# Kernel tuning notes

Hardware: AMD Instinct MI355X
Metric: run time of the kernel (lower is better)

## Reference

```python
import jax, jax.numpy as jnp
import numpy as np

T_HORIZON, S_DIM, A_DIM, H = 65536, 128, 8, 256
GAMMA, LMBDA, EPS_CLIP, VF_COEF, ENT_COEF = 0.99, 0.95, 0.2, 0.5, 0.01
LOG2PI = float(np.log(2.0 * np.pi))


def setup_inputs() -> dict:
    key = jax.random.key(0)
    ks = jax.random.split(key, 24)
    s = jax.random.normal(ks[0], (T_HORIZON, S_DIM), jnp.float32)
    a = jax.random.normal(ks[1], (T_HORIZON, A_DIM), jnp.float32)
    r = jax.random.normal(ks[2], (T_HORIZON, 1), jnp.float32)
    sp = jax.random.normal(ks[3], (T_HORIZON, S_DIM), jnp.float32)
    log_prob_a_old = jax.random.normal(ks[4], (T_HORIZON, 1), jnp.float32)
    d_mask = (jax.random.uniform(ks[5], (T_HORIZON, 1)) > 0.05).astype(jnp.float32)

    def lin(k, fan_in, fan_out, std):
        return jax.random.normal(k, (fan_in, fan_out), jnp.float32) * (std / np.sqrt(fan_in))

    params = dict(
        pi_W1=lin(ks[6], S_DIM, H, np.sqrt(2)), pi_b1=jnp.zeros((H,), jnp.float32),
        pi_W2=lin(ks[7], H, H, np.sqrt(2)),     pi_b2=jnp.zeros((H,), jnp.float32),
        mu_W=lin(ks[8], H, A_DIM, 0.01),        mu_b=jnp.zeros((A_DIM,), jnp.float32),
        log_std=jnp.zeros((A_DIM,), jnp.float32),
        v_W1=lin(ks[9], S_DIM, H, np.sqrt(2)),  v_b1=jnp.zeros((H,), jnp.float32),
        v_W2=lin(ks[10], H, H, np.sqrt(2)),     v_b2=jnp.zeros((H,), jnp.float32),
        vh_W=lin(ks[11], H, 1, 1.0),            vh_b=jnp.zeros((1,), jnp.float32),
    )
    return dict(s=s, a=a, r=r, sp=sp, log_prob_a_old=log_prob_a_old, d_mask=d_mask, **params)


def reference(s, a, r, sp, log_prob_a_old, d_mask,
              pi_W1, pi_b1, pi_W2, pi_b2, mu_W, mu_b, log_std,
              v_W1, v_b1, v_W2, v_b2, vh_W, vh_b):
    def mlp(x, W1, b1, W2, b2):
        return jnp.tanh(jnp.tanh(x @ W1 + b1) @ W2 + b2)

    def v_fn(x):
        return mlp(x, v_W1, v_b1, v_W2, v_b2) @ vh_W + vh_b  # [N, 1]

    # ---- GAE (computed under no_grad in the original) ----
    values = jax.lax.stop_gradient(v_fn(s))                  # [T, 1]
    v_last = jax.lax.stop_gradient(v_fn(sp[-1:]))            # [1, 1]
    next_values = jnp.concatenate([values[1:], v_last], axis=0)
    deltas = r + GAMMA * next_values * d_mask - values       # [T, 1]

    def gae_step(gae, inp):
        delta, m = inp
        gae = delta + GAMMA * LMBDA * m * gae
        return gae, gae

    _, advantages = jax.lax.scan(gae_step, jnp.zeros((1,), deltas.dtype),
                                 (deltas, d_mask), reverse=True)  # [T, 1]
    returns = advantages + values
    advantages = (advantages - advantages.mean()) / (advantages.std(ddof=1) + 1e-8)
    advantages = jax.lax.stop_gradient(advantages)
    returns = jax.lax.stop_gradient(returns)

    # ---- PPO clipped loss (single full-batch pass) ----
    mu = mlp(s, pi_W1, pi_b1, pi_W2, pi_b2) @ mu_W + mu_b    # [T, A]
    std = jnp.exp(log_std)
    log_prob = (-0.5 * ((a - mu) / std) ** 2 - log_std - 0.5 * LOG2PI).sum(-1, keepdims=True)
    ratio = jnp.exp(log_prob - log_prob_a_old)               # [T, 1]
    pg_loss = -jnp.minimum(ratio * advantages,
                           jnp.clip(ratio, 1.0 - EPS_CLIP, 1.0 + EPS_CLIP) * advantages).mean()
    diff = v_fn(s) - returns
    vf_loss = jnp.where(jnp.abs(diff) < 1.0, 0.5 * diff ** 2, jnp.abs(diff) - 0.5).mean()
    entropy = (0.5 + 0.5 * LOG2PI + log_std).mean()          # Normal entropy, constant over batch
    return pg_loss + VF_COEF * vf_loss - ENT_COEF * entropy
```

## Files before the change

kernel.cpp:

```cpp
#include <hip/hip_runtime.h>
#include <math.h>

#define TH 65536
#define SD 128
#define AD 8
#define HD 256

constexpr float GAMMA  = 0.99f;
constexpr float LMBDA  = 0.95f;
constexpr float EPSC   = 0.2f;
constexpr float VFC    = 0.5f;
constexpr float ENTC   = 0.01f;
constexpr float LOG2PI = 1.8378770664093453f;

typedef __attribute__((ext_vector_type(8))) short short8;
typedef __attribute__((ext_vector_type(4))) float f32x4;

constexpr size_t WS_VALUES = 0;
constexpr size_t WS_ADV    = 65540;
constexpr size_t WS_RATIO  = 131080;
constexpr size_t WS_CHP    = 196616;
constexpr size_t WS_CHB    = 196680;
constexpr size_t WS_CARRY  = 196744;
constexpr size_t WS_SCAL   = 196808;
constexpr size_t WS_BF     = 196816;
constexpr size_t SW_PIW1 = 0;
constexpr size_t SW_PIW2 = 32768;
constexpr size_t SW_VW1  = 98304;
constexpr size_t SW_VW2  = 131072;

__device__ __forceinline__ unsigned short f2bf(float x) {
    unsigned int u = __float_as_uint(x);
    unsigned int r = (u + 0x7fffu + ((u >> 16) & 1u)) >> 16;
    return (unsigned short)r;
}

__device__ __forceinline__ float ftanh(float x) {
    float cx = fminf(fmaxf(x, -9.f), 9.f);
    float e = __expf(cx + cx);
    return (e - 1.f) * __builtin_amdgcn_rcpf(e + 1.f);
}

__global__ __launch_bounds__(256) void swizzle_kernel(
    const float* __restrict__ piW1, const float* __restrict__ vW1,
    const float* __restrict__ piW2, const float* __restrict__ vW2,
    unsigned short* __restrict__ dPiW1, unsigned short* __restrict__ dVW1,
    unsigned short* __restrict__ dPiW2, unsigned short* __restrict__ dVW2,
    float* __restrict__ scal)
{
    if (blockIdx.x == 0 && threadIdx.x < 8) scal[threadIdx.x] = 0.f;
    int fid = blockIdx.x * 256 + threadIdx.x;
    const float* S; unsigned short* D; int lo;
    if      (fid <  4096) { S = piW1; D = dPiW1; lo = 0;     }
    else if (fid <  8192) { S = vW1;  D = dVW1;  lo = 4096;  }
    else if (fid < 16384) { S = piW2; D = dPiW2; lo = 8192;  }
    else                  { S = vW2;  D = dVW2;  lo = 16384; }
    int f = fid - lo;
    int lane = f & 63, grp = f >> 6;
    int nt = grp % 16, ks = grp / 16;
    int k0 = ks * 32 + ((lane >> 4) << 3);
    int n  = nt * 16 + (lane & 15);
    unsigned int u[4];
#pragma unroll
    for (int jj = 0; jj < 4; ++jj) {
        float v0 = S[(size_t)(k0 + 2 * jj) * HD + n];
        float v1 = S[(size_t)(k0 + 2 * jj + 1) * HD + n];
        u[jj] = (unsigned int)f2bf(v0) | ((unsigned int)f2bf(v1) << 16);
    }
    ((uint4*)D)[f] = make_uint4(u[0], u[1], u[2], u[3]);
}

template <int NKS, int ASTRIDE>
__device__ __forceinline__ void runlayer(
    f32x4* acc, const unsigned short* __restrict__ Ws,
    const unsigned short* ab, int l15, int quad, int rowgrp, int colhalf, int lane)
{
#pragma unroll
    for (int nt = 0; nt < 8; ++nt) acc[nt] = (f32x4){0.f, 0.f, 0.f, 0.f};
#pragma unroll
    for (int ks = 0; ks < NKS; ++ks) {
        short8 af = *(const short8*)(ab + (rowgrp * 16 + l15) * ASTRIDE + ks * 32 + quad * 8);
#pragma unroll
        for (int ntl = 0; ntl < 8; ++ntl) {
            short8 bf = ((const short8*)Ws)[(ks * 16 + colhalf * 8 + ntl) * 64 + lane];
            acc[ntl] = __builtin_amdgcn_mfma_f32_16x16x32_bf16(af, bf, acc[ntl], 0, 0, 0);
        }
    }
}

__global__ __launch_bounds__(256, 3) void mlp_fused_kernel(
    const float* __restrict__ X, const float* __restrict__ Xlast,
    const unsigned short* __restrict__ piW1s, const float* __restrict__ pib1,
    const unsigned short* __restrict__ piW2s, const float* __restrict__ pib2,
    const float* __restrict__ muW, const float* __restrict__ mub,
    const float* __restrict__ logstd,
    const float* __restrict__ act, const float* __restrict__ lpold,
    const unsigned short* __restrict__ vW1s, const float* __restrict__ vb1,
    const unsigned short* __restrict__ vW2s, const float* __restrict__ vb2,
    const float* __restrict__ vhW, const float* __restrict__ vhb,
    float* __restrict__ values, float* __restrict__ ratio)
{
    __shared__ unsigned short xs[32 * 136];
    __shared__ unsigned short h1[32 * 264];
    __shared__ float cmb[2][32][8];
    const int tid = threadIdx.x;
    const int lane = tid & 63, wave = tid >> 6;
    const int l15 = lane & 15, quad = lane >> 4;
    const int rowgrp = wave >> 1, colhalf = wave & 1;
    const bool vonly = (blockIdx.x == gridDim.x - 1);
    const float* Xp = vonly ? Xlast : X + (size_t)blockIdx.x * 32 * SD;
    const int nrows = vonly ? 1 : 32;
    const int vout0 = vonly ? TH : blockIdx.x * 32;

#pragma unroll
    for (int i = 0; i < 4; ++i) {
        int f = tid + i * 256;
        int rr = f >> 5, c4 = f & 31;
        float4 v = make_float4(0.f, 0.f, 0.f, 0.f);
        if (rr < nrows) v = *(const float4*)(Xp + (size_t)rr * SD + c4 * 4);
        unsigned int u0 = (unsigned int)f2bf(v.x) | ((unsigned int)f2bf(v.y) << 16);
        unsigned int u1 = (unsigned int)f2bf(v.z) | ((unsigned int)f2bf(v.w) << 16);
        *(uint2*)(xs + rr * 136 + c4 * 4) = make_uint2(u0, u1);
    }
    __syncthreads();

    f32x4 acc[8];

    if (!vonly) {
        runlayer<4, 136>(acc, piW1s, xs, l15, quad, rowgrp, colhalf, lane);
#pragma unroll
        for (int ntl = 0; ntl < 8; ++ntl) {
            int col = (colhalf * 8 + ntl) * 16 + l15;
            float bb = pib1[col];
#pragma unroll
            for (int rg = 0; rg < 4; ++rg)
                h1[(rowgrp * 16 + quad * 4 + rg) * 264 + col] = f2bf(ftanh(acc[ntl][rg] + bb));
        }
        __syncthreads();
        runlayer<8, 264>(acc, piW2s, h1, l15, quad, rowgrp, colhalf, lane);
        float pm[4][8];
#pragma unroll
        for (int rg = 0; rg < 4; ++rg)
#pragma unroll
            for (int aj = 0; aj < 8; ++aj) pm[rg][aj] = 0.f;
#pragma unroll
        for (int ntl = 0; ntl < 8; ++ntl) {
            int col = (colhalf * 8 + ntl) * 16 + l15;
            float bb = pib2[col];
            float4 w0 = *(const float4*)(muW + (size_t)col * AD);
            float4 w1 = *(const float4*)(muW + (size_t)col * AD + 4);
            float wv[8] = {w0.x, w0.y, w0.z, w0.w, w1.x, w1.y, w1.z, w1.w};
#pragma unroll
            for (int rg = 0; rg < 4; ++rg) {
                float hv = ftanh(acc[ntl][rg] + bb);
#pragma unroll
                for (int aj = 0; aj < 8; ++aj) pm[rg][aj] = fmaf(hv, wv[aj], pm[rg][aj]);
            }
        }
#pragma unroll
        for (int off = 8; off >= 1; off >>= 1)
#pragma unroll
            for (int rg = 0; rg < 4; ++rg)
#pragma unroll
                for (int aj = 0; aj < 8; ++aj)
                    pm[rg][aj] += __shfl_xor(pm[rg][aj], off, 16);
        if (l15 == 0) {
#pragma unroll
            for (int rg = 0; rg < 4; ++rg) {
                *(float4*)&cmb[colhalf][rowgrp * 16 + quad * 4 + rg][0] =
                    make_float4(pm[rg][0], pm[rg][1], pm[rg][2], pm[rg][3]);
                *(float4*)&cmb[colhalf][rowgrp * 16 + quad * 4 + rg][4] =
                    make_float4(pm[rg][4], pm[rg][5], pm[rg][6], pm[rg][7]);
            }
        }
        __syncthreads();
        if (tid < 32) {
            int row = blockIdx.x * 32 + tid;
            const float* ar = act + (size_t)row * AD;
            float lp = 0.f;
#pragma unroll
            for (int aj = 0; aj < 8; ++aj) {
                float ls = logstd[aj];
                float mu = cmb[0][tid][aj] + cmb[1][tid][aj] + mub[aj];
                float z = (ar[aj] - mu) * __expf(-ls);
                lp += -0.5f * z * z - ls;
            }
            lp -= 4.f * LOG2PI;
            ratio[row] = __expf(lp - lpold[row]);
        }
    }

    runlayer<4, 136>(acc, vW1s, xs, l15, quad, rowgrp, colhalf, lane);
#pragma unroll
    for (int ntl = 0; ntl < 8; ++ntl) {
        int col = (colhalf * 8 + ntl) * 16 + l15;
        float bb = vb1[col];
#pragma unroll
        for (int rg = 0; rg < 4; ++rg)
            h1[(rowgrp * 16 + quad * 4 + rg) * 264 + col] = f2bf(ftanh(acc[ntl][rg] + bb));
    }
    __syncthreads();
    runlayer<8, 264>(acc, vW2s, h1, l15, quad, rowgrp, colhalf, lane);
    float vp[4] = {0.f, 0.f, 0.f, 0.f};
#pragma unroll
    for (int ntl = 0; ntl < 8; ++ntl) {
        int col = (colhalf * 8 + ntl) * 16 + l15;
        float bb = vb2[col], w = vhW[col];
#pragma unroll
        for (int rg = 0; rg < 4; ++rg) vp[rg] += ftanh(acc[ntl][rg] + bb) * w;
    }
#pragma unroll
    for (int off = 8; off >= 1; off >>= 1)
#pragma unroll
        for (int rg = 0; rg < 4; ++rg) vp[rg] += __shfl_xor(vp[rg], off, 16);
    if (l15 == 0) {
#pragma unroll
        for (int rg = 0; rg < 4; ++rg)
            cmb[colhalf][rowgrp * 16 + quad * 4 + rg][0] = vp[rg];
    }
    __syncthreads();
    if (tid < nrows)
        values[vout0 + tid] = cmb[0][tid][0] + cmb[1][tid][0] + vhb[0];
}

__global__ __launch_bounds__(256) void gae_chunk_kernel(
    const float* __restrict__ rw, const float* __restrict__ m,
    const float* __restrict__ values,
    float* __restrict__ chunkP, float* __restrict__ chunkB)
{
    __shared__ float sp_[256], sb_[256];
    const int j = threadIdx.x;
    const int t0 = blockIdx.x * 1024 + j * 4;

    float4 vv = *(const float4*)(values + t0);
    float v4 = values[t0 + 4];
    float4 rr = *(const float4*)(rw + t0);
    float4 mm = *(const float4*)(m + t0);
    float vs[5] = {vv.x, vv.y, vv.z, vv.w, v4};
    float rs[4] = {rr.x, rr.y, rr.z, rr.w};
    float ms[4] = {mm.x, mm.y, mm.z, mm.w};
    float d[4];
#pragma unroll
    for (int i = 0; i < 4; ++i)
        d[i] = rs[i] + GAMMA * vs[i + 1] * ms[i] - vs[i];

    const float g = GAMMA * LMBDA;
    float P = 1.f, B = 0.f;
#pragma unroll
    for (int i = 3; i >= 0; --i) {
        float p = g * ms[i];
        B = d[i] + p * B;
        P = p * P;
    }
    sp_[j] = P; sb_[j] = B;
    __syncthreads();
    for (int dstep = 1; dstep < 256; dstep <<= 1) {
        float pj = sp_[j], bj = sb_[j], pk = 1.f, bk = 0.f;
        if (j + dstep < 256) { pk = sp_[j + dstep]; bk = sb_[j + dstep]; }
        __syncthreads();
        sp_[j] = pj * pk;
        sb_[j] = bj + pj * bk;
        __syncthreads();
    }
    if (j == 0) { chunkP[blockIdx.x] = sp_[0]; chunkB[blockIdx.x] = sb_[0]; }
}

__global__ __launch_bounds__(64) void gae_carry_kernel(
    const float* __restrict__ chunkP, const float* __restrict__ chunkB,
    float* __restrict__ carry)
{
    if (threadIdx.x == 0) {
        float A = 0.f;
        for (int c = 63; c >= 0; --c) {
            carry[c] = A;
            A = chunkB[c] + chunkP[c] * A;
        }
    }
}

__global__ __launch_bounds__(256) void gae_apply_kernel(
    const float* __restrict__ rw, const float* __restrict__ m,
    const float* __restrict__ values, const float* __restrict__ carry,
    float* __restrict__ adv_out, float* __restrict__ scal)
{
    __shared__ float sp_[256], sb_[256];
    __shared__ float red[12];
    const int j = threadIdx.x;
    const int t0 = blockIdx.x * 1024 + j * 4;

    float4 vv = *(const float4*)(values + t0);
    float v4 = values[t0 + 4];
    float4 rr = *(const float4*)(rw + t0);
    float4 mm = *(const float4*)(m + t0);
    float vs[5] = {vv.x, vv.y, vv.z, vv.w, v4};
    float rs[4] = {rr.x, rr.y, rr.z, rr.w};
    float ms[4] = {mm.x, mm.y, mm.z, mm.w};
    float ds[4];
#pragma unroll
    for (int i = 0; i < 4; ++i)
        ds[i] = rs[i] + GAMMA * vs[i + 1] * ms[i] - vs[i];
    const float g = GAMMA * LMBDA;

    float P = 1.f, B = 0.f;
#pragma unroll
    for (int i = 3; i >= 0; --i) {
        float p = g * ms[i];
        B = ds[i] + p * B;
        P = p * P;
    }
    sp_[j] = P; sb_[j] = B;
    __syncthreads();
    for (int dstep = 1; dstep < 256; dstep <<= 1) {
        float pj = sp_[j], bj = sb_[j], pk = 1.f, bk = 0.f;
        if (j + dstep < 256) { pk = sp_[j + dstep]; bk = sb_[j + dstep]; }
        __syncthreads();
        sp_[j] = pj * pk;
        sb_[j] = bj + pj * bk;
        __syncthreads();
    }
    float Pe = 1.f, Be = 0.f;
    if (j < 255) { Pe = sp_[j + 1]; Be = sb_[j + 1]; }
    float A = Be + Pe * carry[blockIdx.x];

    float s1 = 0.f, s2 = 0.f, vf = 0.f;
    float a4[4];
#pragma unroll
    for (int i = 3; i >= 0; --i) {
        A = ds[i] + g * ms[i] * A;
        a4[i] = A;
        float ab = fabsf(A);
        vf += (ab < 1.f) ? 0.5f * A * A : ab - 0.5f;
        s1 += A;
        s2 += A * A;
    }
    *(float4*)(adv_out + t0) = make_float4(a4[0], a4[1], a4[2], a4[3]);

#pragma unroll
    for (int off = 32; off >= 1; off >>= 1) {
        s1 += __shfl_down(s1, off, 64);
        s2 += __shfl_down(s2, off, 64);
        vf += __shfl_down(vf, off, 64);
    }
    if ((j & 63) == 0) {
        int w = j >> 6;
        red[w] = s1; red[4 + w] = s2; red[8 + w] = vf;
    }
    __syncthreads();
    if (j == 0) {
        atomicAdd(&scal[0], red[0] + red[1] + red[2] + red[3]);
        atomicAdd(&scal[1], red[4] + red[5] + red[6] + red[7]);
        atomicAdd(&scal[2], red[8] + red[9] + red[10] + red[11]);
    }
}

__global__ __launch_bounds__(256) void pg_final_kernel(
    const float* __restrict__ ratio, const float* __restrict__ adv,
    float* __restrict__ scal, const float* __restrict__ logstd,
    float* __restrict__ out)
{
    __shared__ float red[4];
    const int tid = threadIdx.x;
    const int t0 = blockIdx.x * 1024 + tid * 4;

    const float ssum = scal[0], ssq = scal[1];
    const float meanA = ssum / (float)TH;
    const float varA = fmaxf((ssq - ssum * ssum / (float)TH) / (float)(TH - 1), 0.f);
    const float inv = 1.f / (sqrtf(varA) + 1e-8f);

    float4 a4 = *(const float4*)(adv + t0);
    float4 r4 = *(const float4*)(ratio + t0);
    float as[4] = {a4.x, a4.y, a4.z, a4.w};
    float rs[4] = {r4.x, r4.y, r4.z, r4.w};
    float pg = 0.f;
#pragma unroll
    for (int i = 0; i < 4; ++i) {
        float aN = (as[i] - meanA) * inv;
        float rc = fminf(fmaxf(rs[i], 1.f - EPSC), 1.f + EPSC);
        pg -= fminf(rs[i] * aN, rc * aN);
    }
#pragma unroll
    for (int off = 32; off >= 1; off >>= 1) pg += __shfl_down(pg, off, 64);
    if ((tid & 63) == 0) red[tid >> 6] = pg;
    __syncthreads();
    if (tid == 0) {
        atomicAdd(&scal[3], red[0] + red[1] + red[2] + red[3]);
        __threadfence();
        float old = atomicAdd(&scal[4], 1.f);
        if (old == 63.f) {
            float pgs = atomicAdd(&scal[3], 0.f);
            float vfs = atomicAdd(&scal[2], 0.f);
            float ls = 0.f;
#pragma unroll
            for (int jj = 0; jj < AD; ++jj) ls += logstd[jj];
            float entropy = 0.5f + 0.5f * LOG2PI + ls / (float)AD;
            out[0] = pgs / (float)TH + VFC * (vfs / (float)TH) - ENTC * entropy;
        }
    }
}

extern "C" void kernel_launch(void* const* d_in, const int* in_sizes, int n_in,
                              void* d_out, int out_size, void* d_ws, size_t ws_size,
                              hipStream_t stream) {
    const float* s      = (const float*)d_in[0];
    const float* a      = (const float*)d_in[1];
    const float* r      = (const float*)d_in[2];
    const float* sp     = (const float*)d_in[3];
    const float* lpold  = (const float*)d_in[4];
    const float* dmask  = (const float*)d_in[5];
    const float* piW1   = (const float*)d_in[6];
    const float* pib1   = (const float*)d_in[7];
    const float* piW2   = (const float*)d_in[8];
    const float* pib2   = (const float*)d_in[9];
    const float* muW    = (const float*)d_in[10];
    const float* mub    = (const float*)d_in[11];
    const float* logstd = (const float*)d_in[12];
    const float* vW1    = (const float*)d_in[13];
    const float* vb1    = (const float*)d_in[14];
    const float* vW2    = (const float*)d_in[15];
    const float* vb2    = (const float*)d_in[16];
    const float* vhW    = (const float*)d_in[17];
    const float* vhb    = (const float*)d_in[18];

    float* ws      = (float*)d_ws;
    float* values  = ws + WS_VALUES;
    float* adv     = ws + WS_ADV;
    float* ratio   = ws + WS_RATIO;
    float* chunkP  = ws + WS_CHP;
    float* chunkB  = ws + WS_CHB;
    float* carry   = ws + WS_CARRY;
    float* scal    = ws + WS_SCAL;
    unsigned short* bfbase = (unsigned short*)(ws + WS_BF);
    unsigned short* dPiW1 = bfbase + SW_PIW1;
    unsigned short* dPiW2 = bfbase + SW_PIW2;
    unsigned short* dVW1  = bfbase + SW_VW1;
    unsigned short* dVW2  = bfbase + SW_VW2;

    swizzle_kernel<<<96, 256, 0, stream>>>(piW1, vW1, piW2, vW2,
                                           dPiW1, dVW1, dPiW2, dVW2, scal);

    mlp_fused_kernel<<<TH / 32 + 1, 256, 0, stream>>>(
        s, sp + (size_t)(TH - 1) * SD,
        dPiW1, pib1, dPiW2, pib2, muW, mub, logstd, a, lpold,
        dVW1, vb1, dVW2, vb2, vhW, vhb,
        values, ratio);

    gae_chunk_kernel<<<64, 256, 0, stream>>>(r, dmask, values, chunkP, chunkB);
    gae_carry_kernel<<<1, 64, 0, stream>>>(chunkP, chunkB, carry);
    gae_apply_kernel<<<64, 256, 0, stream>>>(r, dmask, values, carry, adv, scal);

    pg_final_kernel<<<64, 256, 0, stream>>>(ratio, adv, scal, logstd, (float*)d_out);
}
```

Baseline: 207.1 us.

## Switch MFMA to fp16, coalesce weight swizzle, fuse GAE and loss kernels

Four post-MLP kernels (chunk scan, carry, apply, pg-final) are merged into one 64-block kernel that uses global atomic counters with spin-waits as grid barriers, which removes launch gaps and the advantage round-trip through memory. The MLP switches from bf16 to fp16 MFMA with packed round-toward-zero conversion. The weight swizzle is rewritten to read coalesced float4 rows and scatter 16-bit stores across twice as many blocks. The spin barriers assume all 64 blocks are resident at once, and fp16 changes numerical range and rounding.

```diff
diff --git a/kernel.cpp b/kernel.cpp
--- a/kernel.cpp
+++ b/kernel.cpp
@@ -13,26 +13,24 @@
 constexpr float ENTC   = 0.01f;
 constexpr float LOG2PI = 1.8378770664093453f;
 
-typedef __attribute__((ext_vector_type(8))) short short8;
+typedef _Float16 half8 __attribute__((ext_vector_type(8)));
+typedef __fp16 fp16x2 __attribute__((ext_vector_type(2)));
 typedef __attribute__((ext_vector_type(4))) float f32x4;
 
 constexpr size_t WS_VALUES = 0;
-constexpr size_t WS_ADV    = 65540;
 constexpr size_t WS_RATIO  = 131080;
 constexpr size_t WS_CHP    = 196616;
 constexpr size_t WS_CHB    = 196680;
-constexpr size_t WS_CARRY  = 196744;
-constexpr size_t WS_SCAL   = 196808;
-constexpr size_t WS_BF     = 196816;
+constexpr size_t WS_SCAL   = 196744;
+constexpr size_t WS_BF     = 196752;
 constexpr size_t SW_PIW1 = 0;
 constexpr size_t SW_PIW2 = 32768;
 constexpr size_t SW_VW1  = 98304;
 constexpr size_t SW_VW2  = 131072;
 
-__device__ __forceinline__ unsigned short f2bf(float x) {
-    unsigned int u = __float_as_uint(x);
-    unsigned int r = (u + 0x7fffu + ((u >> 16) & 1u)) >> 16;
-    return (unsigned short)r;
+__device__ __forceinline__ unsigned pk2h(float a, float b) {
+    fp16x2 h = __builtin_amdgcn_cvt_pkrtz(a, b);
+    return __builtin_bit_cast(unsigned, h);
 }
 
 __device__ __forceinline__ float ftanh(float x) {
@@ -49,25 +47,24 @@
     float* __restrict__ scal)
 {
     if (blockIdx.x == 0 && threadIdx.x < 8) scal[threadIdx.x] = 0.f;
-    int fid = blockIdx.x * 256 + threadIdx.x;
+    int g = blockIdx.x * 256 + threadIdx.x;
     const float* S; unsigned short* D; int lo;
-    if      (fid <  4096) { S = piW1; D = dPiW1; lo = 0;     }
-    else if (fid <  8192) { S = vW1;  D = dVW1;  lo = 4096;  }
-    else if (fid < 16384) { S = piW2; D = dPiW2; lo = 8192;  }
-    else                  { S = vW2;  D = dVW2;  lo = 16384; }
-    int f = fid - lo;
-    int lane = f & 63, grp = f >> 6;
-    int nt = grp % 16, ks = grp / 16;
-    int k0 = ks * 32 + ((lane >> 4) << 3);
-    int n  = nt * 16 + (lane & 15);
-    unsigned int u[4];
-#pragma unroll
-    for (int jj = 0; jj < 4; ++jj) {
-        float v0 = S[(size_t)(k0 + 2 * jj) * HD + n];
-        float v1 = S[(size_t)(k0 + 2 * jj + 1) * HD + n];
-        u[jj] = (unsigned int)f2bf(v0) | ((unsigned int)f2bf(v1) << 16);
-    }
-    ((uint4*)D)[f] = make_uint4(u[0], u[1], u[2], u[3]);
+    if      (g <  8192) { S = piW1; D = dPiW1; lo = 0;     }
+    else if (g < 24576) { S = piW2; D = dPiW2; lo = 8192;  }
+    else if (g < 32768) { S = vW1;  D = dVW1;  lo = 24576; }
+    else                { S = vW2;  D = dVW2;  lo = 32768; }
+    int q = g - lo;
+    int k = q >> 6, n4 = (q & 63) * 4;
+    float4 v = *(const float4*)(S + (size_t)k * HD + n4);
+    int ks = k >> 5, kq = (k >> 3) & 3, j = k & 7;
+    int nt = n4 >> 4, nr = n4 & 15;
+    unsigned short* base = D + ((size_t)(ks * 16 + nt) * 64 + kq * 16 + nr) * 8 + j;
+    unsigned p01 = pk2h(v.x, v.y);
+    unsigned p23 = pk2h(v.z, v.w);
+    base[0]  = (unsigned short)(p01 & 0xffff);
+    base[8]  = (unsigned short)(p01 >> 16);
+    base[16] = (unsigned short)(p23 & 0xffff);
+    base[24] = (unsigned short)(p23 >> 16);
 }
 
 template <int NKS, int ASTRIDE>
@@ -79,13 +76,23 @@
     for (int nt = 0; nt < 8; ++nt) acc[nt] = (f32x4){0.f, 0.f, 0.f, 0.f};
 #pragma unroll
     for (int ks = 0; ks < NKS; ++ks) {
-        short8 af = *(const short8*)(ab + (rowgrp * 16 + l15) * ASTRIDE + ks * 32 + quad * 8);
+        half8 af = *(const half8*)(ab + (rowgrp * 16 + l15) * ASTRIDE + ks * 32 + quad * 8);
 #pragma unroll
         for (int ntl = 0; ntl < 8; ++ntl) {
-            short8 bf = ((const short8*)Ws)[(ks * 16 + colhalf * 8 + ntl) * 64 + lane];
-            acc[ntl] = __builtin_amdgcn_mfma_f32_16x16x32_bf16(af, bf, acc[ntl], 0, 0, 0);
-        }
-    }
+            half8 bf = ((const half8*)Ws)[(ks * 16 + colhalf * 8 + ntl) * 64 + lane];
+            acc[ntl] = __builtin_amdgcn_mfma_f32_16x16x32_f16(af, bf, acc[ntl], 0, 0, 0);
+        }
+    }
+}
+
+__device__ __forceinline__ void store4(unsigned short* dst, int stride,
+                                       float t0, float t1, float t2, float t3)
+{
+    unsigned p01 = pk2h(t0, t1), p23 = pk2h(t2, t3);
+    dst[0]          = (unsigned short)(p01 & 0xffff);
+    dst[stride]     = (unsigned short)(p01 >> 16);
+    dst[2 * stride] = (unsigned short)(p23 & 0xffff);
+    dst[3 * stride] = (unsigned short)(p23 >> 16);
 }
 
 __global__ __launch_bounds__(256, 3) void mlp_fused_kernel(
@@ -118,9 +125,7 @@
         int rr = f >> 5, c4 = f & 31;
         float4 v = make_float4(0.f, 0.f, 0.f, 0.f);
         if (rr < nrows) v = *(const float4*)(Xp + (size_t)rr * SD + c4 * 4);
-        unsigned int u0 = (unsigned int)f2bf(v.x) | ((unsigned int)f2bf(v.y) << 16);
-        unsigned int u1 = (unsigned int)f2bf(v.z) | ((unsigned int)f2bf(v.w) << 16);
-        *(uint2*)(xs + rr * 136 + c4 * 4) = make_uint2(u0, u1);
+        *(uint2*)(xs + rr * 136 + c4 * 4) = make_uint2(pk2h(v.x, v.y), pk2h(v.z, v.w));
     }
     __syncthreads();
 
@@ -132,9 +137,9 @@
         for (int ntl = 0; ntl < 8; ++ntl) {
             int col = (colhalf * 8 + ntl) * 16 + l15;
             float bb = pib1[col];
-#pragma unroll
-            for (int rg = 0; rg < 4; ++rg)
-                h1[(rowgrp * 16 + quad * 4 + rg) * 264 + col] = f2bf(ftanh(acc[ntl][rg] + bb));
+            store4(&h1[(rowgrp * 16 + quad * 4) * 264 + col], 264,
+                   ftanh(acc[ntl][0] + bb), ftanh(acc[ntl][1] + bb),
+                   ftanh(acc[ntl][2] + bb), ftanh(acc[ntl][3] + bb));
         }
         __syncthreads();
         runlayer<8, 264>(acc, piW2s, h1, l15, quad, rowgrp, colhalf, lane);
@@ -195,9 +200,9 @@
     for (int ntl = 0; ntl < 8; ++ntl) {
         int col = (colhalf * 8 + ntl) * 16 + l15;
         float bb = vb1[col];
-#pragma unroll
-        for (int rg = 0; rg < 4; ++rg)
-            h1[(rowgrp * 16 + quad * 4 + rg) * 264 + col] = f2bf(ftanh(acc[ntl][rg] + bb));
+        store4(&h1[(rowgrp * 16 + quad * 4) * 264 + col], 264,
+               ftanh(acc[ntl][0] + bb), ftanh(acc[ntl][1] + bb),
+               ftanh(acc[ntl][2] + bb), ftanh(acc[ntl][3] + bb));
     }
     __syncthreads();
     runlayer<8, 264>(acc, vW2s, h1, l15, quad, rowgrp, colhalf, lane);
@@ -223,70 +228,20 @@
         values[vout0 + tid] = cmb[0][tid][0] + cmb[1][tid][0] + vhb[0];
 }
 
-__global__ __launch_bounds__(256) void gae_chunk_kernel(
+__global__ __launch_bounds__(256) void gae_fused_kernel(
     const float* __restrict__ rw, const float* __restrict__ m,
-    const float* __restrict__ values,
-    float* __restrict__ chunkP, float* __restrict__ chunkB)
+    const float* __restrict__ values, const float* __restrict__ ratio,
+    const float* __restrict__ logstd,
+    float* __restrict__ chunkP, float* __restrict__ chunkB,
+    float* __restrict__ scal, float* __restrict__ out)
 {
     __shared__ float sp_[256], sb_[256];
+    __shared__ float cp[64], cb[64];
+    __shared__ float red[12];
+    __shared__ float bcast[4];
     const int j = threadIdx.x;
     const int t0 = blockIdx.x * 1024 + j * 4;
-
-    float4 vv = *(const float4*)(values + t0);
-    float v4 = values[t0 + 4];
-    float4 rr = *(const float4*)(rw + t0);
-    float4 mm = *(const float4*)(m + t0);
-    float vs[5] = {vv.x, vv.y, vv.z, vv.w, v4};
-    float rs[4] = {rr.x, rr.y, rr.z, rr.w};
-    float ms[4] = {mm.x, mm.y, mm.z, mm.w};
-    float d[4];
-#pragma unroll
-    for (int i = 0; i < 4; ++i)
-        d[i] = rs[i] + GAMMA * vs[i + 1] * ms[i] - vs[i];
-
     const float g = GAMMA * LMBDA;
-    float P = 1.f, B = 0.f;
-#pragma unroll
-    for (int i = 3; i >= 0; --i) {
-        float p = g * ms[i];
-        B = d[i] + p * B;
-        P = p * P;
-    }
-    sp_[j] = P; sb_[j] = B;
-    __syncthreads();
-    for (int dstep = 1; dstep < 256; dstep <<= 1) {
-        float pj = sp_[j], bj = sb_[j], pk = 1.f, bk = 0.f;
-        if (j + dstep < 256) { pk = sp_[j + dstep]; bk = sb_[j + dstep]; }
-        __syncthreads();
-        sp_[j] = pj * pk;
-        sb_[j] = bj + pj * bk;
-        __syncthreads();
-    }
-    if (j == 0) { chunkP[blockIdx.x] = sp_[0]; chunkB[blockIdx.x] = sb_[0]; }
-}
-
-__global__ __launch_bounds__(64) void gae_carry_kernel(
-    const float* __restrict__ chunkP, const float* __restrict__ chunkB,
-    float* __restrict__ carry)
-{
-    if (threadIdx.x == 0) {
-        float A = 0.f;
-        for (int c = 63; c >= 0; --c) {
-            carry[c] = A;
-            A = chunkB[c] + chunkP[c] * A;
-        }
-    }
-}
-
-__global__ __launch_bounds__(256) void gae_apply_kernel(
-    const float* __restrict__ rw, const float* __restrict__ m,
-    const float* __restrict__ values, const float* __restrict__ carry,
-    float* __restrict__ adv_out, float* __restrict__ scal)
-{
-    __shared__ float sp_[256], sb_[256];
-    __shared__ float red[12];
-    const int j = threadIdx.x;
-    const int t0 = blockIdx.x * 1024 + j * 4;
 
     float4 vv = *(const float4*)(values + t0);
     float v4 = values[t0 + 4];
@@ -299,7 +254,6 @@
 #pragma unroll
     for (int i = 0; i < 4; ++i)
         ds[i] = rs[i] + GAMMA * vs[i + 1] * ms[i] - vs[i];
-    const float g = GAMMA * LMBDA;
 
     float P = 1.f, B = 0.f;
 #pragma unroll
@@ -318,10 +272,30 @@
         sb_[j] = bj + pj * bk;
         __syncthreads();
     }
+    if (j == 0) {
+        atomicExch(&chunkP[blockIdx.x], sp_[0]);
+        atomicExch(&chunkB[blockIdx.x], sb_[0]);
+        __threadfence();
+        atomicAdd(&scal[5], 1.f);
+        while (atomicAdd(&scal[5], 0.f) < 64.f) __builtin_amdgcn_s_sleep(2);
+    }
+    __syncthreads();
+    if (j < 64) {
+        cp[j] = atomicAdd(&chunkP[j], 0.f);
+        cb[j] = atomicAdd(&chunkB[j], 0.f);
+    }
+    __syncthreads();
+    if (j == 0) {
+        float A = 0.f;
+        for (int c = 63; c > (int)blockIdx.x; --c) A = cb[c] + cp[c] * A;
+        bcast[0] = A;
+    }
+    __syncthreads();
+    const float carry = bcast[0];
+
     float Pe = 1.f, Be = 0.f;
     if (j < 255) { Pe = sp_[j + 1]; Be = sb_[j + 1]; }
-    float A = Be + Pe * carry[blockIdx.x];
-
+    float A = Be + Pe * carry;
     float s1 = 0.f, s2 = 0.f, vf = 0.f;
     float a4[4];
 #pragma unroll
@@ -333,8 +307,6 @@
         s1 += A;
         s2 += A * A;
     }
-    *(float4*)(adv_out + t0) = make_float4(a4[0], a4[1], a4[2], a4[3]);
-
 #pragma unroll
     for (int off = 32; off >= 1; off >>= 1) {
         s1 += __shfl_down(s1, off, 64);
@@ -350,39 +322,33 @@
         atomicAdd(&scal[0], red[0] + red[1] + red[2] + red[3]);
         atomicAdd(&scal[1], red[4] + red[5] + red[6] + red[7]);
         atomicAdd(&scal[2], red[8] + red[9] + red[10] + red[11]);
-    }
-}
-
-__global__ __launch_bounds__(256) void pg_final_kernel(
-    const float* __restrict__ ratio, const float* __restrict__ adv,
-    float* __restrict__ scal, const float* __restrict__ logstd,
-    float* __restrict__ out)
-{
-    __shared__ float red[4];
-    const int tid = threadIdx.x;
-    const int t0 = blockIdx.x * 1024 + tid * 4;
-
-    const float ssum = scal[0], ssq = scal[1];
+        __threadfence();
+        atomicAdd(&scal[6], 1.f);
+        while (atomicAdd(&scal[6], 0.f) < 64.f) __builtin_amdgcn_s_sleep(2);
+        bcast[1] = atomicAdd(&scal[0], 0.f);
+        bcast[2] = atomicAdd(&scal[1], 0.f);
+    }
+    __syncthreads();
+
+    const float ssum = bcast[1], ssq = bcast[2];
     const float meanA = ssum / (float)TH;
     const float varA = fmaxf((ssq - ssum * ssum / (float)TH) / (float)(TH - 1), 0.f);
     const float inv = 1.f / (sqrtf(varA) + 1e-8f);
 
-    float4 a4 = *(const float4*)(adv + t0);
     float4 r4 = *(const float4*)(ratio + t0);
-    float as[4] = {a4.x, a4.y, a4.z, a4.w};
-    float rs[4] = {r4.x, r4.y, r4.z, r4.w};
+    float rt[4] = {r4.x, r4.y, r4.z, r4.w};
     float pg = 0.f;
 #pragma unroll
     for (int i = 0; i < 4; ++i) {
-        float aN = (as[i] - meanA) * inv;
-        float rc = fminf(fmaxf(rs[i], 1.f - EPSC), 1.f + EPSC);
-        pg -= fminf(rs[i] * aN, rc * aN);
+        float aN = (a4[i] - meanA) * inv;
+        float rc = fminf(fmaxf(rt[i], 1.f - EPSC), 1.f + EPSC);
+        pg -= fminf(rt[i] * aN, rc * aN);
     }
 #pragma unroll
     for (int off = 32; off >= 1; off >>= 1) pg += __shfl_down(pg, off, 64);
-    if ((tid & 63) == 0) red[tid >> 6] = pg;
-    __syncthreads();
-    if (tid == 0) {
+    if ((j & 63) == 0) red[j >> 6] = pg;
+    __syncthreads();
+    if (j == 0) {
         atomicAdd(&scal[3], red[0] + red[1] + red[2] + red[3]);
         __threadfence();
         float old = atomicAdd(&scal[4], 1.f);
@@ -423,11 +389,9 @@
 
     float* ws      = (float*)d_ws;
     float* values  = ws + WS_VALUES;
-    float* adv     = ws + WS_ADV;
     float* ratio   = ws + WS_RATIO;
     float* chunkP  = ws + WS_CHP;
     float* chunkB  = ws + WS_CHB;
-    float* carry   = ws + WS_CARRY;
     float* scal    = ws + WS_SCAL;
     unsigned short* bfbase = (unsigned short*)(ws + WS_BF);
     unsigned short* dPiW1 = bfbase + SW_PIW1;
@@ -435,8 +399,8 @@
     unsigned short* dVW1  = bfbase + SW_VW1;
     unsigned short* dVW2  = bfbase + SW_VW2;
 
-    swizzle_kernel<<<96, 256, 0, stream>>>(piW1, vW1, piW2, vW2,
-                                           dPiW1, dVW1, dPiW2, dVW2, scal);
+    swizzle_kernel<<<192, 256, 0, stream>>>(piW1, vW1, piW2, vW2,
+                                            dPiW1, dVW1, dPiW2, dVW2, scal);
 
     mlp_fused_kernel<<<TH / 32 + 1, 256, 0, stream>>>(
         s, sp + (size_t)(TH - 1) * SD,
@@ -444,9 +408,6 @@
         dVW1, vb1, dVW2, vb2, vhW, vhb,
         values, ratio);
 
-    gae_chunk_kernel<<<64, 256, 0, stream>>>(r, dmask, values, chunkP, chunkB);
-    gae_carry_kernel<<<1, 64, 0, stream>>>(chunkP, chunkB, carry);
-    gae_apply_kernel<<<64, 256, 0, stream>>>(r, dmask, values, carry, adv, scal);
-
-    pg_final_kernel<<<64, 256, 0, stream>>>(ratio, adv, scal, logstd, (float*)d_out);
-}
+    gae_fused_kernel<<<64, 256, 0, stream>>>(r, dmask, values, ratio, logstd,
+                                             chunkP, chunkB, scal, (float*)d_out);
+}
```

New measurement: 209.1 us. About the same (+1.0%).
